# Optimization experiments

Hardware: AMD Instinct MI355X
Metric: run time of the kernel (lower is better)

The kernel has to match this reference:

```python
import jax, jax.numpy as jnp
import numpy as np

HARRIS_K = 0.04
SOBEL_SCALE = 1.0 / 12.0  # OpenCV: 1/((1<<(ksize-1))*blockSize) = 1/(4*3) for float input
THRESH_FRAC = 0.7

_DX = jnp.array([[-1., 0., 1.], [-2., 0., 2.], [-1., 0., 1.]], dtype=jnp.float32)
_DY = _DX.T
_BOX = jnp.ones((3, 3), dtype=jnp.float32)  # unnormalized 3x3 box sum (blockSize=3)


def _filt3(img, k):
    # img: (N,1,H,W); reflect-101 pad (OpenCV BORDER_DEFAULT) then valid cross-correlation
    p = jnp.pad(img, ((0, 0), (0, 0), (1, 1), (1, 1)), mode='reflect')
    return jax.lax.conv_general_dilated(
        p, k.reshape(1, 1, 3, 3), (1, 1), 'VALID',
        dimension_numbers=('NCHW', 'OIHW', 'NCHW'))


def harris_mask(x):
    # x: (B,C,H,W) -> binary-ish corner mask, same shape
    B, C, H, W = x.shape
    img = x.reshape(B * C, 1, H, W)
    dx = _filt3(img, _DX) * SOBEL_SCALE
    dy = _filt3(img, _DY) * SOBEL_SCALE
    ixx = _filt3(dx * dx, _BOX)
    ixy = _filt3(dx * dy, _BOX)
    iyy = _filt3(dy * dy, _BOX)
    R = (ixx * iyy - ixy * ixy) - HARRIS_K * (ixx + iyy) ** 2
    # cv2.dilate(dst, None): 3x3 max filter (border does not contribute)
    dst = jax.lax.reduce_window(R, -jnp.inf, jax.lax.max,
                                (1, 1, 3, 3), (1, 1, 1, 1), 'SAME')
    t = THRESH_FRAC * jnp.max(dst, axis=(2, 3), keepdims=True)
    # >t -> 1, <t -> 0, ==t -> keep original pixel (exactly as the torch code does)
    mask = jnp.where(dst > t, 1.0, jnp.where(dst < t, 0.0, img))
    return mask.reshape(B, C, H, W)


def setup_inputs() -> dict:
    key = jax.random.key(0)
    k1, k2, k3 = jax.random.split(key, 3)
    B, C, H, W = 8, 64, 256, 256
    x = jax.random.normal(k1, (B, C, H, W), dtype=jnp.float32)
    weight = jax.random.normal(k2, (C, C, 1, 1), dtype=jnp.float32) * (1.0 / np.sqrt(C))
    bias = jax.random.normal(k3, (C,), dtype=jnp.float32) * 0.01
    return {"x": x, "weight": weight, "bias": bias}


def reference(x, weight, bias):
    # y = ReLU(Conv1x1(x))
    y = jax.lax.conv_general_dilated(
        x, weight, (1, 1), 'VALID',
        dimension_numbers=('NCHW', 'OIHW', 'NCHW')) + bias[None, :, None, None]
    y = jax.nn.relu(y)
    att = harris_mask(x)  # computed via numpy in original -> no grad path
    return att * y + x
```

## Files before the change

### kernel.cpp

```cpp
#include <hip/hip_runtime.h>

#define HH 256
#define WW 256
#define BATCH 8
#define CH 64
#define NIMG (BATCH*CH)
#define HWSZ (HH*WW)
#define SCL (1.0f/12.0f)
#define KH 0.04f
#define TFRAC 0.7f
#define RS 16
#define NEGINF (-__builtin_inff())

__global__ __launch_bounds__(256) void k1(const float* __restrict__ x,
                                          float* __restrict__ rv,
                                          float* __restrict__ ms)
{
    const int tid = threadIdx.x;
    const int img = blockIdx.x >> 2;
    const int tx  = tid & 63;
    const int sy  = ((blockIdx.x & 3) << 2) | (tid >> 6);
    const int r0  = sy * RS;
    const int c0  = tx * 4;
    const float* ib = x + (size_t)img * HWSZ;
    float* rb = rv + (size_t)img * HWSZ;

    float im[3][8];
    float hx[3][4], hq[3][4], hy[3][4];
    float R[3][4];
    float rmax = NEGINF;

    auto loadrow = [&](int gr, float* d) {
        gr = gr < 0 ? -gr : (gr >= HH ? 2*HH - 2 - gr : gr);
        float4 own = *(const float4*)(ib + gr * WW + c0);
        float upz = __shfl_up(own.z, 1);
        float upw = __shfl_up(own.w, 1);
        float dnx = __shfl_down(own.x, 1);
        float dny = __shfl_down(own.y, 1);
        d[0] = (tx > 0)  ? upz : own.z;
        d[1] = (tx > 0)  ? upw : own.y;
        d[2] = own.x; d[3] = own.y; d[4] = own.z; d[5] = own.w;
        d[6] = (tx < 63) ? dnx : own.z;
        d[7] = (tx < 63) ? dny : own.y;
    };

    loadrow(r0 - 3, im[0]);
    loadrow(r0 - 2, im[1]);

#pragma unroll
    for (int i = 0; i < RS + 4; ++i) {
        const int m = r0 - 2 + i;
        loadrow(m + 1, im[(2 + i) % 3]);

        {
            const int ia = i % 3, ib2 = (i + 1) % 3, ic = (i + 2) % 3;
            float t1[8], t2[8];
#pragma unroll
            for (int q = 0; q < 8; ++q) {
                t1[q] = im[ia][q] + 2.0f * im[ib2][q] + im[ic][q];
                t2[q] = im[ic][q] - im[ia][q];
            }
            float pxv[6], pqv[6], pyv[6];
#pragma unroll
            for (int q = 0; q < 6; ++q) {
                float dx = SCL * (t1[q + 2] - t1[q]);
                float dy = SCL * (t2[q] + 2.0f * t2[q + 1] + t2[q + 2]);
                pxv[q] = dx * dx;
                pqv[q] = dx * dy;
                pyv[q] = dy * dy;
            }
            if (tx == 0)  pqv[0] = -pqv[0];
            if (tx == 63) pqv[5] = -pqv[5];
            const int po = i % 3;
#pragma unroll
            for (int j = 0; j < 4; ++j) {
                hx[po][j] = pxv[j] + pxv[j + 1] + pxv[j + 2];
                hq[po][j] = pqv[j] + pqv[j + 1] + pqv[j + 2];
                hy[po][j] = pyv[j] + pyv[j + 1] + pyv[j + 2];
            }
        }

        if (i >= 2) {
            const int s = m - 1;
            const int A = (i + 1) % 3, B2 = (i + 2) % 3, C2 = i % 3;
            const bool vs = (s >= 0) && (s < HH);
#pragma unroll
            for (int j = 0; j < 4; ++j) {
                float ixx, ixy, iyy;
                if (s == 0) {
                    ixx = hx[B2][j] + 2.0f * hx[C2][j];
                    ixy = hq[B2][j] + 2.0f * hq[C2][j];
                    iyy = hy[B2][j] + 2.0f * hy[C2][j];
                } else if (s == HH - 1) {
                    ixx = 2.0f * hx[A][j] + hx[B2][j];
                    ixy = 2.0f * hq[A][j] + hq[B2][j];
                    iyy = 2.0f * hy[A][j] + hy[B2][j];
                } else {
                    ixx = hx[A][j] + hx[B2][j] + hx[C2][j];
                    ixy = hq[A][j] + hq[B2][j] + hq[C2][j];
                    iyy = hy[A][j] + hy[B2][j] + hy[C2][j];
                }
                float tr = ixx + iyy;
                float Rj = (ixx * iyy - ixy * ixy) - KH * tr * tr;
                Rj = vs ? Rj : NEGINF;
                R[i % 3][j] = Rj;
                rmax = fmaxf(rmax, Rj);
            }
        }

        if (i >= 4) {
            const int r = r0 - 4 + i;
            const int A = (i + 1) % 3, B2 = (i + 2) % 3, C2 = i % 3;
            float4 o;
            o.x = fmaxf(fmaxf(R[A][0], R[B2][0]), R[C2][0]);
            o.y = fmaxf(fmaxf(R[A][1], R[B2][1]), R[C2][1]);
            o.z = fmaxf(fmaxf(R[A][2], R[B2][2]), R[C2][2]);
            o.w = fmaxf(fmaxf(R[A][3], R[B2][3]), R[C2][3]);
            *(float4*)(rb + r * WW + c0) = o;
        }
    }

#pragma unroll
    for (int off = 32; off; off >>= 1) rmax = fmaxf(rmax, __shfl_xor(rmax, off));
    __shared__ float sm[4];
    if ((tid & 63) == 0) sm[tid >> 6] = rmax;
    __syncthreads();
    if (tid == 0) {
        float mm = fmaxf(fmaxf(sm[0], sm[1]), fmaxf(sm[2], sm[3]));
        ms[(img << 2) | (blockIdx.x & 3)] = mm;
    }
}

__global__ __launch_bounds__(512, 4) void k2(const float* __restrict__ x,
                                             const float* __restrict__ wgt,
                                             const float* __restrict__ bias,
                                             const float* __restrict__ ms,
                                             float* __restrict__ io)
{
    __shared__ __align__(16) float Xl[CH][WW];
    __shared__ __align__(16) float Wl[CH][CH];
    __shared__ float tmax[CH];
    const int tid = threadIdx.x;
    const int wv  = tid >> 6;
    const int l   = tid & 63;
    const int b   = blockIdx.x >> 8;
    const int h   = blockIdx.x & 255;
    const int oc0 = wv << 3;

    {
        const float* xrow = x + (size_t)b * CH * HWSZ + (size_t)h * WW + (l << 2);
        float4 tmp[8];
#pragma unroll
        for (int k = 0; k < 8; ++k)
            tmp[k] = *(const float4*)(xrow + (size_t)(oc0 + k) * HWSZ);
#pragma unroll
        for (int k = 0; k < 8; ++k)
            *(float4*)&Xl[oc0 + k][l << 2] = tmp[k];

        const float4* wg4 = (const float4*)wgt;
        float4* wl4 = (float4*)&Wl[0][0];
        float4 w0 = wg4[tid], w1 = wg4[tid + 512];
        wl4[tid] = w0; wl4[tid + 512] = w1;

        if (tid < CH) {
            float4 m4 = *(const float4*)(ms + ((b * CH + tid) << 2));
            tmax[tid] = TFRAC * fmaxf(fmaxf(m4.x, m4.y), fmaxf(m4.z, m4.w));
        }
    }
    __syncthreads();

    float acc[8][4];
#pragma unroll
    for (int j = 0; j < 8; ++j) {
        const float bj = bias[oc0 + j];
        acc[j][0] = bj; acc[j][1] = bj; acc[j][2] = bj; acc[j][3] = bj;
    }
#pragma unroll 4
    for (int c2 = 0; c2 < CH; c2 += 2) {
        const float4 xa = *(const float4*)&Xl[c2][l << 2];
        const float4 xb = *(const float4*)&Xl[c2 + 1][l << 2];
#pragma unroll
        for (int j = 0; j < 8; ++j) {
            const float2 wj = *(const float2*)&Wl[oc0 + j][c2];
            acc[j][0] = fmaf(wj.x, xa.x, acc[j][0]);
            acc[j][1] = fmaf(wj.x, xa.y, acc[j][1]);
            acc[j][2] = fmaf(wj.x, xa.z, acc[j][2]);
            acc[j][3] = fmaf(wj.x, xa.w, acc[j][3]);
            acc[j][0] = fmaf(wj.y, xb.x, acc[j][0]);
            acc[j][1] = fmaf(wj.y, xb.y, acc[j][1]);
            acc[j][2] = fmaf(wj.y, xb.z, acc[j][2]);
            acc[j][3] = fmaf(wj.y, xb.w, acc[j][3]);
        }
    }

    const size_t pb = (size_t)b * CH * HWSZ + (size_t)h * WW + (size_t)(l << 2);
    float4 rvv[8];
#pragma unroll
    for (int j = 0; j < 8; ++j)
        rvv[j] = *(const float4*)(io + pb + (size_t)(oc0 + j) * HWSZ);

#pragma unroll
    for (int j = 0; j < 8; ++j) {
        const int c = oc0 + j;
        float lf = __shfl_up(rvv[j].w, 1);
        float rt = __shfl_down(rvv[j].x, 1);
        if (l == 0)  lf = NEGINF;
        if (l == 63) rt = NEGINF;
        const float d0 = fmaxf(fmaxf(lf,       rvv[j].x), rvv[j].y);
        const float d1 = fmaxf(fmaxf(rvv[j].x, rvv[j].y), rvv[j].z);
        const float d2 = fmaxf(fmaxf(rvv[j].y, rvv[j].z), rvv[j].w);
        const float d3 = fmaxf(fmaxf(rvv[j].z, rvv[j].w), rt);
        const float t = tmax[c];
        const float4 xi = *(const float4*)&Xl[c][l << 2];
        const float y0 = fmaxf(acc[j][0], 0.0f);
        const float y1 = fmaxf(acc[j][1], 0.0f);
        const float y2 = fmaxf(acc[j][2], 0.0f);
        const float y3 = fmaxf(acc[j][3], 0.0f);
        float4 o;
        o.x = fmaf(d0 > t ? 1.0f : (d0 < t ? 0.0f : xi.x), y0, xi.x);
        o.y = fmaf(d1 > t ? 1.0f : (d1 < t ? 0.0f : xi.y), y1, xi.y);
        o.z = fmaf(d2 > t ? 1.0f : (d2 < t ? 0.0f : xi.z), y2, xi.z);
        o.w = fmaf(d3 > t ? 1.0f : (d3 < t ? 0.0f : xi.w), y3, xi.w);
        *(float4*)(io + pb + (size_t)c * HWSZ) = o;
    }
}

extern "C" void kernel_launch(void* const* d_in, const int* in_sizes, int n_in,
                              void* d_out, int out_size, void* d_ws, size_t ws_size,
                              hipStream_t stream)
{
    const float* x    = (const float*)d_in[0];
    const float* wgt  = (const float*)d_in[1];
    const float* bias = (const float*)d_in[2];
    float* out = (float*)d_out;
    float* ms = (float*)d_ws;

    hipLaunchKernelGGL(k1, dim3(NIMG * 4), dim3(256), 0, stream, x, out, ms);
    hipLaunchKernelGGL(k2, dim3(BATCH * HH), dim3(512), 0, stream,
                       x, wgt, bias, ms, out);
}
```

Before: 329.0 us.

## Prefetch rows in Harris pass, async LDS loads and scalar weights in conv pass

Result: faster. 307.3 us (-6.6%).

```diff
diff --git a/kernel.cpp b/kernel.cpp
--- a/kernel.cpp
+++ b/kernel.cpp
@@ -30,9 +30,11 @@
     float R[3][4];
     float rmax = NEGINF;
 
-    auto loadrow = [&](int gr, float* d) {
+    auto loadraw = [&](int gr) -> float4 {
         gr = gr < 0 ? -gr : (gr >= HH ? 2*HH - 2 - gr : gr);
-        float4 own = *(const float4*)(ib + gr * WW + c0);
+        return *(const float4*)(ib + gr * WW + c0);
+    };
+    auto expand = [&](float4 own, float* d) {
         float upz = __shfl_up(own.z, 1);
         float upw = __shfl_up(own.w, 1);
         float dnx = __shfl_down(own.x, 1);
@@ -44,13 +46,15 @@
         d[7] = (tx < 63) ? dny : own.y;
     };
 
-    loadrow(r0 - 3, im[0]);
-    loadrow(r0 - 2, im[1]);
+    expand(loadraw(r0 - 3), im[0]);
+    expand(loadraw(r0 - 2), im[1]);
+    float4 raw = loadraw(r0 - 1);
 
 #pragma unroll
     for (int i = 0; i < RS + 4; ++i) {
         const int m = r0 - 2 + i;
-        loadrow(m + 1, im[(2 + i) % 3]);
+        expand(raw, im[(2 + i) % 3]);
+        if (i < RS + 3) raw = loadraw(m + 2);
 
         {
             const int ia = i % 3, ib2 = (i + 1) % 3, ic = (i + 2) % 3;
@@ -138,30 +142,23 @@
                                              float* __restrict__ io)
 {
     __shared__ __align__(16) float Xl[CH][WW];
-    __shared__ __align__(16) float Wl[CH][CH];
     __shared__ float tmax[CH];
     const int tid = threadIdx.x;
     const int wv  = tid >> 6;
     const int l   = tid & 63;
     const int b   = blockIdx.x >> 8;
     const int h   = blockIdx.x & 255;
-    const int oc0 = wv << 3;
+    const int oc0 = __builtin_amdgcn_readfirstlane(wv << 3);
 
     {
         const float* xrow = x + (size_t)b * CH * HWSZ + (size_t)h * WW + (l << 2);
-        float4 tmp[8];
-#pragma unroll
-        for (int k = 0; k < 8; ++k)
-            tmp[k] = *(const float4*)(xrow + (size_t)(oc0 + k) * HWSZ);
-#pragma unroll
-        for (int k = 0; k < 8; ++k)
-            *(float4*)&Xl[oc0 + k][l << 2] = tmp[k];
-
-        const float4* wg4 = (const float4*)wgt;
-        float4* wl4 = (float4*)&Wl[0][0];
-        float4 w0 = wg4[tid], w1 = wg4[tid + 512];
-        wl4[tid] = w0; wl4[tid + 512] = w1;
-
+#pragma unroll
+        for (int k = 0; k < 8; ++k) {
+            __builtin_amdgcn_global_load_lds(
+                (const __attribute__((address_space(1))) unsigned int*)(xrow + (size_t)(oc0 + k) * HWSZ),
+                (__attribute__((address_space(3))) unsigned int*)&Xl[oc0 + k][0],
+                16, 0, 0);
+        }
         if (tid < CH) {
             float4 m4 = *(const float4*)(ms + ((b * CH + tid) << 2));
             tmax[tid] = TFRAC * fmaxf(fmaxf(m4.x, m4.y), fmaxf(m4.z, m4.w));
@@ -169,19 +166,27 @@
     }
     __syncthreads();
 
+    const size_t pb = (size_t)b * CH * HWSZ + (size_t)h * WW + (size_t)(l << 2);
+    float4 rvv[8];
+#pragma unroll
+    for (int j = 0; j < 8; ++j)
+        rvv[j] = *(const float4*)(io + pb + (size_t)(oc0 + j) * HWSZ);
+
     float acc[8][4];
 #pragma unroll
     for (int j = 0; j < 8; ++j) {
         const float bj = bias[oc0 + j];
         acc[j][0] = bj; acc[j][1] = bj; acc[j][2] = bj; acc[j][3] = bj;
     }
-#pragma unroll 4
-    for (int c2 = 0; c2 < CH; c2 += 2) {
-        const float4 xa = *(const float4*)&Xl[c2][l << 2];
-        const float4 xb = *(const float4*)&Xl[c2 + 1][l << 2];
+#pragma unroll 2
+    for (int c4 = 0; c4 < CH; c4 += 4) {
+        const float4 xa = *(const float4*)&Xl[c4][l << 2];
+        const float4 xb = *(const float4*)&Xl[c4 + 1][l << 2];
+        const float4 xc = *(const float4*)&Xl[c4 + 2][l << 2];
+        const float4 xd = *(const float4*)&Xl[c4 + 3][l << 2];
 #pragma unroll
         for (int j = 0; j < 8; ++j) {
-            const float2 wj = *(const float2*)&Wl[oc0 + j][c2];
+            const float4 wj = *(const float4*)(wgt + (oc0 + j) * CH + c4);
             acc[j][0] = fmaf(wj.x, xa.x, acc[j][0]);
             acc[j][1] = fmaf(wj.x, xa.y, acc[j][1]);
             acc[j][2] = fmaf(wj.x, xa.z, acc[j][2]);
@@ -190,14 +195,16 @@
             acc[j][1] = fmaf(wj.y, xb.y, acc[j][1]);
             acc[j][2] = fmaf(wj.y, xb.z, acc[j][2]);
             acc[j][3] = fmaf(wj.y, xb.w, acc[j][3]);
-        }
-    }
-
-    const size_t pb = (size_t)b * CH * HWSZ + (size_t)h * WW + (size_t)(l << 2);
-    float4 rvv[8];
-#pragma unroll
-    for (int j = 0; j < 8; ++j)
-        rvv[j] = *(const float4*)(io + pb + (size_t)(oc0 + j) * HWSZ);
+            acc[j][0] = fmaf(wj.z, xc.x, acc[j][0]);
+            acc[j][1] = fmaf(wj.z, xc.y, acc[j][1]);
+            acc[j][2] = fmaf(wj.z, xc.z, acc[j][2]);
+            acc[j][3] = fmaf(wj.z, xc.w, acc[j][3]);
+            acc[j][0] = fmaf(wj.w, xd.x, acc[j][0]);
+            acc[j][1] = fmaf(wj.w, xd.y, acc[j][1]);
+            acc[j][2] = fmaf(wj.w, xd.z, acc[j][2]);
+            acc[j][3] = fmaf(wj.w, xd.w, acc[j][3]);
+        }
+    }
 
 #pragma unroll
     for (int j = 0; j < 8; ++j) {
```
